# Optimization experiments

Hardware: AMD Instinct MI355X
Metric: run time of the kernel (lower is better)

## Reference

```python
import jax, jax.numpy as jnp
import numpy as np

WS = 8  # window/grid size, hard-coded in GlobalCirculationBlock
NH = 8  # num_heads


def _ln(x, w, b):
    m = jnp.mean(x, -1, keepdims=True)
    v = jnp.mean((x - m) ** 2, -1, keepdims=True)
    return (x - m) * jax.lax.rsqrt(v + 1e-5) * w + b


def _attn(q, k, v, scale):
    # q,k,v: [..., S, hd]
    s = jnp.einsum('...qd,...kd->...qk', q, k) * scale
    return jnp.einsum('...qk,...kd->...qd', jax.nn.softmax(s, axis=-1), v)


def setup_inputs() -> dict:
    key = jax.random.key(0)
    ks = jax.random.split(key, 8)
    B, C, H, W = 8, 128, 128, 128
    hid = 4 * C
    f = lambda k, shape, s=0.02: jax.random.normal(k, shape, jnp.float32) * s
    z = lambda n: jnp.zeros((n,), jnp.float32)
    return {
        'x': f(ks[0], (B, C, H, W), 1.0),
        'conv_w': f(ks[1], (C, 1, 3, 3)),        # depthwise 3x3 pos embed
        'conv_b': z(C),
        'norm1_w': jnp.ones((C,), jnp.float32), 'norm1_b': z(C),
        'wqkv': f(ks[2], (C, 3 * C)),            # qkv_bias=False
        'proj_w': f(ks[3], (C, C)), 'proj_b': z(C),
        'norm2_w': jnp.ones((C,), jnp.float32), 'norm2_b': z(C),
        'fc1_w': f(ks[4], (C, hid)), 'fc1_b': z(hid),
        'fc2_w': f(ks[5], (hid, C)), 'fc2_b': z(C),
        'ls1': jnp.full((C,), 1e-2, jnp.float32),
        'ls2': jnp.full((C,), 1e-2, jnp.float32),
    }


def reference(x, conv_w, conv_b, norm1_w, norm1_b, wqkv, proj_w, proj_b,
              norm2_w, norm2_b, fc1_w, fc1_b, fc2_w, fc2_b, ls1, ls2):
    B, C, H, W = x.shape
    nh, ws = NH, WS
    hd = C // nh
    scale = hd ** -0.5
    nhl = nh // 2                     # local heads == global heads
    nH, nW = H // ws, W // ws         # H,W multiples of ws -> no padding

    # depthwise conv positional embedding + residual
    pos = jax.lax.conv_general_dilated(
        x, conv_w, (1, 1), 'SAME',
        dimension_numbers=('NCHW', 'OIHW', 'NCHW'), feature_group_count=C)
    x = x + pos + conv_b[None, :, None, None]

    xt = x.reshape(B, C, H * W).transpose(0, 2, 1)   # [B, N, C]

    # ---- dual-scale attention ----
    xn = _ln(xt, norm1_w, norm1_b).reshape(B, H, W, C)
    qkv = (xn @ wqkv).reshape(B, H, W, 3, nh, hd)
    q, k, v = qkv[:, :, :, 0], qkv[:, :, :, 1], qkv[:, :, :, 2]  # [B,H,W,nh,hd]

    # local branch: first nhl heads, window attention (seq = ws*ws)
    def win(t):  # [B,H,W,nhl,hd] -> [B,nH,nW,nhl,ws*ws,hd]
        t = t.reshape(B, nH, ws, nW, ws, nhl, hd)
        return t.transpose(0, 1, 3, 5, 2, 4, 6).reshape(B, nH, nW, nhl, ws * ws, hd)

    ol = _attn(win(q[..., :nhl, :]), win(k[..., :nhl, :]), win(v[..., :nhl, :]), scale)
    ol = (ol.reshape(B, nH, nW, nhl, ws, ws, hd)
            .transpose(0, 1, 4, 2, 5, 3, 6)
            .reshape(B, H, W, nhl * hd))

    # global branch: last nhl heads, grid attention (seq = nH*nW)
    def grd(t):  # [B,H,W,nhl,hd] -> [B,ws,ws,nhl,nH*nW,hd]
        t = t.reshape(B, nH, ws, nW, ws, nhl, hd)
        return t.transpose(0, 2, 4, 5, 1, 3, 6).reshape(B, ws, ws, nhl, nH * nW, hd)

    og = _attn(grd(q[..., nhl:, :]), grd(k[..., nhl:, :]), grd(v[..., nhl:, :]), scale)
    og = (og.reshape(B, ws, ws, nhl, nH, nW, hd)
            .transpose(0, 4, 1, 5, 2, 3, 6)
            .reshape(B, H, W, nhl * hd))

    a = jnp.concatenate([ol, og], axis=-1).reshape(B, H * W, C)
    a = a @ proj_w + proj_b
    xt = xt + ls1 * a

    # ---- MLP ----
    h = _ln(xt, norm2_w, norm2_b)
    h = jax.nn.gelu(h @ fc1_w + fc1_b, approximate=False) @ fc2_w + fc2_b
    xt = xt + ls2 * h

    return xt.transpose(0, 2, 1).reshape(B, C, H, W)
```

## Files before the change

kernel.cpp:

```cpp
#include <hip/hip_runtime.h>
#include <hip/hip_bf16.h>

typedef __hip_bfloat16 bf16;
typedef __attribute__((ext_vector_type(8))) short short8;
typedef __attribute__((ext_vector_type(4))) short short4v;
typedef __attribute__((ext_vector_type(4))) float floatx4;
typedef __attribute__((ext_vector_type(16))) float floatx16;

#define Bn 8
#define Cc 128
#define Hh 128
#define Wl 128
#define HW (Hh*Wl)
#define NT (Bn*HW)
#define REG 8388608

#define QSCALE 0.36067376022224085f
#if __has_builtin(__builtin_amdgcn_exp2f)
#define EXP2(x) __builtin_amdgcn_exp2f(x)
#else
#define EXP2(x) __expf((x)*0.69314718055994531f)
#endif

__device__ __forceinline__ float b2f(bf16 v){ return __bfloat162float(v); }
__device__ __forceinline__ bf16  f2b(float v){ return __float2bfloat16(v); }

#define GL16(gp, lp) __builtin_amdgcn_global_load_lds( \
    (__attribute__((address_space(1))) unsigned int*)(gp), \
    (__attribute__((address_space(3))) unsigned int*)(lp), 16, 0, 0)

__global__ __launch_bounds__(256) void transpose_all(const float* __restrict__ wqkv,
                                                     const float* __restrict__ proj_w,
                                                     const float* __restrict__ fc1_w,
                                                     const float* __restrict__ fc2_w,
                                                     bf16* __restrict__ qkvT,
                                                     bf16* __restrict__ projT,
                                                     bf16* __restrict__ fc1T,
                                                     bf16* __restrict__ fc2T){
  int idx = blockIdx.x*256 + threadIdx.x;
  const float* src; bf16* dst; int K, N;
  if(idx < 49152){ src=wqkv; dst=qkvT; K=128; N=384; }
  else if(idx < 65536){ idx -= 49152; src=proj_w; dst=projT; K=128; N=128; }
  else if(idx < 131072){ idx -= 65536; src=fc1_w; dst=fc1T; K=128; N=512; }
  else { idx -= 131072; src=fc2_w; dst=fc2T; K=512; N=128; }
  int n = idx % N, k = idx / N;
  dst[(size_t)n*K + k] = f2b(src[idx]);
}

__global__ __launch_bounds__(256) void conv_kernel(const float* __restrict__ x,
                                                   const float* __restrict__ cw,
                                                   const float* __restrict__ cb,
                                                   float* __restrict__ xt){
  __shared__ float tile[16][132];
  int blk = blockIdx.x;
  int h = blk & 127; int t = blk >> 7;
  int cg = t & 7;    int b = t >> 3;
  int w4 = threadIdx.x & 31;
  int ci = threadIdx.x >> 5;
  int w0 = w4*4;
#pragma unroll
  for(int cc=0; cc<2; cc++){
    int c = cg*16 + ci*2 + cc;
    const float* xp = x + ((size_t)(b*Cc + c))*HW;
    float wg[9];
#pragma unroll
    for(int i=0;i<9;i++) wg[i] = cw[c*9+i];
    float4 rowv[3]; float lf[3], rt[3];
#pragma unroll
    for(int r=0;r<3;r++){
      int hh = h-1+r;
      float4 v = {0.f,0.f,0.f,0.f};
      if(hh>=0 && hh<Hh) v = *(const float4*)(xp + hh*Wl + w0);
      rowv[r] = v;
      float l = __shfl_up(v.w, 1, 32);
      float rr = __shfl_down(v.x, 1, 32);
      lf[r] = (w4==0)  ? 0.f : l;
      rt[r] = (w4==31) ? 0.f : rr;
    }
    float acc0 = cb[c], acc1 = cb[c], acc2 = cb[c], acc3 = cb[c];
#pragma unroll
    for(int r=0;r<3;r++){
      float4 v = rowv[r];
      acc0 += wg[r*3+0]*lf[r] + wg[r*3+1]*v.x + wg[r*3+2]*v.y;
      acc1 += wg[r*3+0]*v.x   + wg[r*3+1]*v.y + wg[r*3+2]*v.z;
      acc2 += wg[r*3+0]*v.y   + wg[r*3+1]*v.z + wg[r*3+2]*v.w;
      acc3 += wg[r*3+0]*v.z   + wg[r*3+1]*v.w + wg[r*3+2]*rt[r];
    }
    acc0 += rowv[1].x; acc1 += rowv[1].y; acc2 += rowv[1].z; acc3 += rowv[1].w;
    float4 o = {acc0, acc1, acc2, acc3};
    *(float4*)&tile[ci*2+cc][w0] = o;
  }
  __syncthreads();
  const size_t obase = ((size_t)b*HW + (size_t)h*Wl)*Cc + cg*16;
#pragma unroll
  for(int i=0;i<8;i++){
    int idx = i*256 + threadIdx.x;
    int c2 = idx & 15, w2 = idx >> 4;
    xt[obase + (size_t)w2*Cc + c2] = tile[c2][w2];
  }
}

__global__ __launch_bounds__(256) void ln_kernel(const float* __restrict__ xt,
                                                 const float* __restrict__ wv,
                                                 const float* __restrict__ bv,
                                                 bf16* __restrict__ xn){
  int tok  = blockIdx.x*4 + (threadIdx.x>>6);
  int lane = threadIdx.x & 63;
  const float* row = xt + (size_t)tok*Cc;
  float v0 = row[lane], v1 = row[lane+64];
  float s = v0+v1;
#pragma unroll
  for(int off=32; off; off>>=1) s += __shfl_down(s, off, 64);
  s = __shfl(s, 0, 64);
  float m = s * (1.0f/128.0f);
  float d0 = v0-m, d1 = v1-m;
  float vs = d0*d0 + d1*d1;
#pragma unroll
  for(int off=32; off; off>>=1) vs += __shfl_down(vs, off, 64);
  vs = __shfl(vs, 0, 64);
  float rstd = rsqrtf(vs*(1.0f/128.0f) + 1e-5f);
  bf16* orow = xn + (size_t)tok*Cc;
  orow[lane]    = f2b(d0*rstd*wv[lane]    + bv[lane]);
  orow[lane+64] = f2b(d1*rstd*wv[lane+64] + bv[lane+64]);
}

template<int EPI>
__global__ __launch_bounds__(256) void mfma_gemm(const bf16* __restrict__ A,
                                                 const bf16* __restrict__ Wt,
                                                 const float* __restrict__ bias,
                                                 bf16* __restrict__ outb,
                                                 float* __restrict__ xt,
                                                 const float* __restrict__ ls,
                                                 int N, int K){
  __shared__ short As[2][128*32];
  __shared__ short Bs[2][64*32];
  const int tid  = threadIdx.x;
  const int lane = tid & 63;
  const int w    = tid >> 6;

  const int nwg = gridDim.x * gridDim.y;
  const int lin = blockIdx.y * gridDim.x + blockIdx.x;
  const int t   = (lin & 7) * (nwg >> 3) + (lin >> 3);
  const int m0  = (t / gridDim.x) * 128;
  const int n0  = (t % gridDim.x) * 64;

  const int l1 = tid + 256;
  const bf16* gA0 = A  + (size_t)(m0 + ((tid>>6)<<4) + (tid&15))*K + (((tid>>4)&3)<<3);
  const bf16* gA1 = A  + (size_t)(m0 + ((l1 >>6)<<4) + (l1 &15))*K + (((l1 >>4)&3)<<3);
  const bf16* gB  = Wt + (size_t)(n0 + ((tid>>6)<<4) + (tid&15))*K + (((tid>>4)&3)<<3);
  const int ldsA0 = w*512;
  const int ldsA1 = 2048 + w*512;
  const int ldsB  = w*512;

  floatx4 acc[4][2];
#pragma unroll
  for(int i=0;i<4;i++)
#pragma unroll
    for(int j=0;j<2;j++) acc[i][j] = (floatx4){0.f,0.f,0.f,0.f};

  const int nk = K >> 5;
  GL16(gA0, &As[0][ldsA0]);
  GL16(gA1, &As[0][ldsA1]);
  GL16(gB , &Bs[0][ldsB ]);
  __syncthreads();

  int cur = 0;
  for(int it=0; it<nk; ++it){
    if(it+1 < nk){
      const int kn = (it+1) << 5;
      GL16(gA0 + kn, &As[cur^1][ldsA0]);
      GL16(gA1 + kn, &As[cur^1][ldsA1]);
      GL16(gB  + kn, &Bs[cur^1][ldsB ]);
    }
    short8 af[4], bfr[2];
#pragma unroll
    for(int mt=0;mt<4;mt++) af[mt] = *(short8*)&As[cur][(((w&1)*4+mt)*64 + lane)*8];
#pragma unroll
    for(int nt=0;nt<2;nt++) bfr[nt] = *(short8*)&Bs[cur][(((w>>1)*2+nt)*64 + lane)*8];
#pragma unroll
    for(int mt=0;mt<4;mt++)
#pragma unroll
      for(int nt=0;nt<2;nt++)
        acc[mt][nt] = __builtin_amdgcn_mfma_f32_16x16x32_bf16(af[mt], bfr[nt], acc[mt][nt], 0, 0, 0);
    __syncthreads();
    cur ^= 1;
  }

#pragma unroll
  for(int mt=0;mt<4;mt++){
#pragma unroll
    for(int nt=0;nt<2;nt++){
#pragma unroll
      for(int r=0;r<4;r++){
        int row = m0 + (w&1)*64 + mt*16 + ((lane>>4))*4 + r;
        int col = n0 + (w>>1)*32 + nt*16 + (lane&15);
        float v = acc[mt][nt][r];
        if(EPI==0){
          int reg = col >> 6;
          int head = (col >> 4) & 3;
          int ch = col & 15;
          int b = row >> 14, h = (row >> 7) & 127, ww = row & 127;
          if(reg < 2) v *= QSCALE;
          size_t didx;
          if(!(reg & 1)){
            int inst = ((b*16 + (h>>3))*16 + (ww>>3))*4 + head;
            int pos = (h&7)*8 + (ww&7);
            didx = ((size_t)inst*64 + pos)*16 + ch;
          } else {
            int inst = ((b*8 + (h&7))*8 + (ww&7))*4 + head;
            int pos = (h>>3)*16 + (ww>>3);
            didx = ((size_t)inst*256 + pos)*16 + ch;
          }
          outb[(size_t)reg*REG + didx] = f2b(v);
        } else if(EPI==1){
          v += bias[col];
          v = 0.5f*v*(1.0f + erff(v*0.70710678118f));
          outb[(size_t)row*N + col] = f2b(v);
        } else if(EPI==2){
          v += bias[col];
          xt[(size_t)row*128 + col] += ls[col]*v;
        } else {
          v += bias[col];
          float rr = xt[(size_t)row*128 + col] + ls[col]*v;
          outb[(size_t)row*128 + col] = f2b(rr);
        }
      }
    }
  }
}

__global__ __launch_bounds__(256) void attn_local2(const bf16* __restrict__ qL,
                                                   const bf16* __restrict__ kL,
                                                   const bf16* __restrict__ vL,
                                                   bf16* __restrict__ a){
  __shared__ short vt[16*72];
  __shared__ short pb[4][16*72];
  const int tid = threadIdx.x;
  const int w = tid >> 6, lane = tid & 63;
  const int n16 = lane & 15, quad = lane >> 4;
  const int blk = blockIdx.x;
  const int head = blk & 3, winid = blk >> 2;
  const bf16* Qb = qL + (size_t)blk*1024;
  const bf16* Kb = kL + (size_t)blk*1024;
  const bf16* Vb = vL + (size_t)blk*1024;

  if(tid < 128){
    int tok = tid >> 1, u = tid & 1;
    short8 v = *(const short8*)(Vb + tok*16 + u*8);
#pragma unroll
    for(int i=0;i<8;i++) vt[(u*8+i)*72 + tok] = ((short*)&v)[i];
  }
  __syncthreads();

  const int qt = w;
  short8 qf = {0,0,0,0,0,0,0,0};
  if(quad < 2) qf = *(const short8*)(Qb + (qt*16+n16)*16 + quad*8);

  floatx4 sf[4];
#pragma unroll
  for(int kt=0; kt<4; kt++){
    short8 kf = {0,0,0,0,0,0,0,0};
    if(quad < 2) kf = *(const short8*)(Kb + (kt*16+n16)*16 + quad*8);
    floatx4 z = (floatx4){0.f,0.f,0.f,0.f};
    sf[kt] = __builtin_amdgcn_mfma_f32_16x16x32_bf16(qf, kf, z, 0, 0, 0);
  }

  float mx[4] = {-1e30f,-1e30f,-1e30f,-1e30f};
#pragma unroll
  for(int kt=0; kt<4; kt++)
#pragma unroll
    for(int r=0;r<4;r++) mx[r] = fmaxf(mx[r], sf[kt][r]);
#pragma unroll
  for(int r=0;r<4;r++){
    mx[r] = fmaxf(mx[r], __shfl_xor(mx[r], 1, 64));
    mx[r] = fmaxf(mx[r], __shfl_xor(mx[r], 2, 64));
    mx[r] = fmaxf(mx[r], __shfl_xor(mx[r], 4, 64));
    mx[r] = fmaxf(mx[r], __shfl_xor(mx[r], 8, 64));
    mx[r] = -mx[r];
  }
  float l[4] = {0.f,0.f,0.f,0.f};
#pragma unroll
  for(int kt=0; kt<4; kt++){
#pragma unroll
    for(int r=0;r<4;r++){
      float p = EXP2(sf[kt][r] + mx[r]);
      l[r] += p;
      bf16 pbv = f2b(p);
      pb[w][(quad*4+r)*72 + kt*16 + n16] = *(short*)&pbv;
    }
  }
#pragma unroll
  for(int r=0;r<4;r++){
    l[r] += __shfl_xor(l[r], 1, 64);
    l[r] += __shfl_xor(l[r], 2, 64);
    l[r] += __shfl_xor(l[r], 4, 64);
    l[r] += __shfl_xor(l[r], 8, 64);
  }

  floatx4 of = (floatx4){0.f,0.f,0.f,0.f};
#pragma unroll
  for(int kb=0; kb<2; kb++){
    short8 pf = *(short8*)&pb[w][n16*72 + kb*32 + quad*8];
    short8 vfb = *(short8*)&vt[n16*72 + kb*32 + quad*8];
    of = __builtin_amdgcn_mfma_f32_16x16x32_bf16(pf, vfb, of, 0, 0, 0);
  }

  const int wj = winid & 15, wi = (winid >> 4) & 15, b = winid >> 8;
  const int ooff = head*16;
#pragma unroll
  for(int r=0;r<4;r++){
    int pos = qt*16 + quad*4 + r;
    int h = wi*8 + (pos>>3), ww = wj*8 + (pos&7);
    size_t t = (size_t)b*HW + (size_t)h*Wl + ww;
    a[t*Cc + ooff + n16] = f2b(of[r] / l[r]);
  }
}

__global__ __launch_bounds__(256) void attn_grid2(const bf16* __restrict__ qG,
                                                  const bf16* __restrict__ kG,
                                                  const bf16* __restrict__ vG,
                                                  bf16* __restrict__ a){
  __shared__ short vt[16*264];
  __shared__ short pb[4][32*136];
  const int tid = threadIdx.x;
  const int w = tid >> 6, lane = tid & 63;
  const int n16 = lane & 15, quad = lane >> 4;
  const int q32 = lane & 31, hb = lane >> 5;
  const int blk = blockIdx.x;
  const int head = blk & 3, ginst = blk >> 2;
  const bf16* Qb = qG + (size_t)blk*4096;
  const bf16* Kb = kG + (size_t)blk*4096;
  const bf16* Vb = vG + (size_t)blk*4096;

#pragma unroll
  for(int it=0; it<2; it++){
    int chunk = it*256 + tid;
    int tok = chunk >> 1, u = chunk & 1;
    short8 v = *(const short8*)(Vb + tok*16 + u*8);
#pragma unroll
    for(int i=0;i<8;i++) vt[(u*8+i)*264 + tok] = ((short*)&v)[i];
  }
  __syncthreads();

  const int sj = ginst & 7, si = (ginst >> 3) & 7, b = ginst >> 6;
  const int ooff = 64 + head*16;
  short* pbw = pb[w];
  const floatx16 Z16 = {0.f,0.f,0.f,0.f,0.f,0.f,0.f,0.f,0.f,0.f,0.f,0.f,0.f,0.f,0.f,0.f};

#pragma unroll
  for(int qi=0; qi<2; qi++){
    const int q0 = w*64 + qi*32;
    const short8 qf = *(const short8*)(Qb + (size_t)(q0 + q32)*16 + hb*8);
    float l_acc = 0.f;
    floatx4 of0 = (floatx4){0.f,0.f,0.f,0.f};
    floatx4 of1 = (floatx4){0.f,0.f,0.f,0.f};
#pragma unroll
    for(int kc=0; kc<2; kc++){
#pragma unroll
      for(int kt=0; kt<4; kt++){
        short8 kf = *(const short8*)(Kb + (size_t)(kc*128 + kt*32 + q32)*16 + hb*8);
        floatx16 s = __builtin_amdgcn_mfma_f32_32x32x16_bf16(kf, qf, Z16, 0, 0, 0);
#pragma unroll
        for(int g=0; g<4; g++){
          float p0 = EXP2(s[4*g+0]);
          float p1 = EXP2(s[4*g+1]);
          float p2 = EXP2(s[4*g+2]);
          float p3 = EXP2(s[4*g+3]);
          l_acc += (p0+p1)+(p2+p3);
          short4v pk = { (short)__bfloat16_as_ushort(f2b(p0)),
                         (short)__bfloat16_as_ushort(f2b(p1)),
                         (short)__bfloat16_as_ushort(f2b(p2)),
                         (short)__bfloat16_as_ushort(f2b(p3)) };
          *(short4v*)&pbw[q32*136 + kt*32 + g*8 + hb*4] = pk;
        }
      }
#pragma unroll
      for(int kb=0; kb<4; kb++){
        short8 vf  = *(short8*)&vt[n16*264 + kc*128 + kb*32 + quad*8];
        short8 pf0 = *(short8*)&pbw[n16*136 + kb*32 + quad*8];
        of0 = __builtin_amdgcn_mfma_f32_16x16x32_bf16(pf0, vf, of0, 0, 0, 0);
        short8 pf1 = *(short8*)&pbw[(16+n16)*136 + kb*32 + quad*8];
        of1 = __builtin_amdgcn_mfma_f32_16x16x32_bf16(pf1, vf, of1, 0, 0, 0);
      }
    }
    l_acc += __shfl_xor(l_acc, 32, 64);
#pragma unroll
    for(int hf=0; hf<2; hf++){
      floatx4 of = hf ? of1 : of0;
#pragma unroll
      for(int r=0;r<4;r++){
        float lr = __shfl(l_acc, hf*16 + quad*4 + r, 64);
        int pos = q0 + hf*16 + quad*4 + r;
        int h = (pos>>4)*8 + si, ww = (pos&15)*8 + sj;
        size_t t = (size_t)b*HW + (size_t)h*Wl + ww;
        a[t*Cc + ooff + n16] = f2b(of[r] / lr);
      }
    }
  }
}

__global__ __launch_bounds__(256) void transpose_kernel(const bf16* __restrict__ xf,
                                                        float* __restrict__ out){
  __shared__ bf16 tile[32][33];
  int t0 = blockIdx.x*32, c0 = blockIdx.y*32, b = blockIdx.z;
  int x = threadIdx.x, y = threadIdx.y;
  const bf16* src = xf + (size_t)b*HW*Cc;
  float* dst = out + (size_t)b*Cc*HW;
#pragma unroll
  for(int i=0;i<4;i++)
    tile[y*4+i][x] = src[(size_t)(t0 + y*4+i)*Cc + c0 + x];
  __syncthreads();
#pragma unroll
  for(int i=0;i<4;i++)
    dst[(size_t)(c0 + y*4+i)*HW + t0 + x] = b2f(tile[x][y*4+i]);
}

extern "C" void kernel_launch(void* const* d_in, const int* in_sizes, int n_in,
                              void* d_out, int out_size, void* d_ws, size_t ws_size,
                              hipStream_t stream) {
  const float* x       = (const float*)d_in[0];
  const float* conv_w  = (const float*)d_in[1];
  const float* conv_b  = (const float*)d_in[2];
  const float* norm1_w = (const float*)d_in[3];
  const float* norm1_b = (const float*)d_in[4];
  const float* wqkv    = (const float*)d_in[5];
  const float* proj_w  = (const float*)d_in[6];
  const float* proj_b  = (const float*)d_in[7];
  const float* norm2_w = (const float*)d_in[8];
  const float* norm2_b = (const float*)d_in[9];
  const float* fc1_w   = (const float*)d_in[10];
  const float* fc1_b   = (const float*)d_in[11];
  const float* fc2_w   = (const float*)d_in[12];
  const float* fc2_b   = (const float*)d_in[13];
  const float* ls1     = (const float*)d_in[14];
  const float* ls2     = (const float*)d_in[15];
  float* out = (float*)d_out;

  char* ws = (char*)d_ws;
  float* xt = (float*)ws;
  bf16*  sh = (bf16*)(ws + (size_t)NT*Cc*4);
  bf16*  qh = (bf16*)(ws + (size_t)NT*Cc*4 + (size_t)NT*Cc*2);
  bf16*  wt = (bf16*)(ws + (size_t)NT*Cc*4 + (size_t)NT*Cc*2 + (size_t)NT*512*2);
  bf16* qkvT = wt;
  bf16* projT= wt + 49152;
  bf16* fc1T = wt + 65536;
  bf16* fc2T = wt + 131072;

  transpose_all<<<196608/256, 256, 0, stream>>>(wqkv, proj_w, fc1_w, fc2_w,
                                                qkvT, projT, fc1T, fc2T);
  conv_kernel<<<Bn*8*Hh, 256, 0, stream>>>(x, conv_w, conv_b, xt);
  ln_kernel<<<NT/4, 256, 0, stream>>>(xt, norm1_w, norm1_b, sh);
  mfma_gemm<0><<<dim3(384/64, NT/128), 256, 0, stream>>>(sh, qkvT, nullptr, qh, nullptr, nullptr, 384, 128);
  attn_grid2<<<2048, 256, 0, stream>>>(qh + (size_t)1*REG, qh + (size_t)3*REG, qh + (size_t)5*REG, sh);
  attn_local2<<<8192, 256, 0, stream>>>(qh + (size_t)0*REG, qh + (size_t)2*REG, qh + (size_t)4*REG, sh);
  mfma_gemm<2><<<dim3(128/64, NT/128), 256, 0, stream>>>(sh, projT, proj_b, nullptr, xt, ls1, 128, 128);
  ln_kernel<<<NT/4, 256, 0, stream>>>(xt, norm2_w, norm2_b, sh);
  mfma_gemm<1><<<dim3(512/64, NT/128), 256, 0, stream>>>(sh, fc1T, fc1_b, qh, nullptr, nullptr, 512, 128);
  mfma_gemm<3><<<dim3(128/64, NT/128), 256, 0, stream>>>(qh, fc2T, fc2_b, sh, xt, ls2, 128, 512);
  transpose_kernel<<<dim3(HW/32, Cc/32, Bn), dim3(32,8), 0, stream>>>(sh, out);
}
```

Measured before the change: 468.8 us.

## Fuse fc1, GELU and fc2 into one MLP kernel keeping hidden in LDS

Replaces the separate fc1+GELU and fc2+residual GEMM launches with one kernel. Each block keeps its 128-row A tile in registers, computes 64-column chunks of the hidden activation into shared memory, and accumulates fc2 immediately. This avoids writing and re-reading the 512-wide hidden tensor through global memory. It also swaps exact erf GELU for a tanh-style approximation using exp2, which adds small numerical error.

```diff
diff --git a/kernel.cpp b/kernel.cpp
--- a/kernel.cpp
+++ b/kernel.cpp
@@ -212,18 +212,123 @@
             didx = ((size_t)inst*256 + pos)*16 + ch;
           }
           outb[(size_t)reg*REG + didx] = f2b(v);
-        } else if(EPI==1){
-          v += bias[col];
-          v = 0.5f*v*(1.0f + erff(v*0.70710678118f));
-          outb[(size_t)row*N + col] = f2b(v);
         } else if(EPI==2){
           v += bias[col];
           xt[(size_t)row*128 + col] += ls[col]*v;
-        } else {
-          v += bias[col];
-          float rr = xt[(size_t)row*128 + col] + ls[col]*v;
-          outb[(size_t)row*128 + col] = f2b(rr);
         }
+      }
+    }
+  }
+}
+
+__global__ __launch_bounds__(256) void fused_mlp(const bf16* A,
+                                                 const bf16* __restrict__ W1,
+                                                 const float* __restrict__ b1,
+                                                 const bf16* __restrict__ W2,
+                                                 const float* __restrict__ b2,
+                                                 const float* __restrict__ xt,
+                                                 const float* __restrict__ ls,
+                                                 bf16* outb){
+  __shared__ short W1s[16*512];
+  __shared__ short W2s[16*512];
+  __shared__ short hs[4][32*72];
+  const int tid = threadIdx.x, lane = tid & 63, w = tid >> 6;
+  const int n16 = lane & 15, quad = lane >> 4;
+  const int lin = blockIdx.x;
+  const int t = (lin & 7)*128 + (lin >> 3);
+  const int m0 = t*128;
+  const int mw = m0 + w*32;
+
+  short8 areg[2][4];
+#pragma unroll
+  for(int mt=0;mt<2;mt++)
+#pragma unroll
+    for(int ks=0;ks<4;ks++)
+      areg[mt][ks] = *(const short8*)(A + (size_t)(mw + mt*16 + n16)*128 + ks*32 + quad*8);
+
+  floatx4 acc2[2][8];
+#pragma unroll
+  for(int i=0;i<2;i++)
+#pragma unroll
+    for(int j=0;j<8;j++) acc2[i][j] = (floatx4){0.f,0.f,0.f,0.f};
+
+  short* hw = hs[w];
+
+  for(int nc=0; nc<8; ++nc){
+    if(nc) __syncthreads();
+#pragma unroll
+    for(int p=0;p<4;p++){
+      int fid = p*4 + w;
+      int nt = fid >> 2, ks = fid & 3;
+      const bf16* s1 = W1 + (size_t)(nc*64 + nt*16 + n16)*128 + ks*32 + quad*8;
+      GL16(s1, &W1s[fid*512]);
+      int nt2 = fid >> 1, ks2 = fid & 1;
+      const bf16* s2 = W2 + (size_t)(nt2*16 + n16)*512 + nc*64 + ks2*32 + quad*8;
+      GL16(s2, &W2s[fid*512]);
+    }
+    __syncthreads();
+
+    floatx4 acc1[2][4];
+#pragma unroll
+    for(int i=0;i<2;i++)
+#pragma unroll
+      for(int j=0;j<4;j++) acc1[i][j] = (floatx4){0.f,0.f,0.f,0.f};
+#pragma unroll
+    for(int ks=0;ks<4;ks++){
+      short8 bfr[4];
+#pragma unroll
+      for(int nt=0;nt<4;nt++) bfr[nt] = *(short8*)&W1s[(nt*4+ks)*512 + lane*8];
+#pragma unroll
+      for(int mt=0;mt<2;mt++)
+#pragma unroll
+        for(int nt=0;nt<4;nt++)
+          acc1[mt][nt] = __builtin_amdgcn_mfma_f32_16x16x32_bf16(areg[mt][ks], bfr[nt], acc1[mt][nt], 0, 0, 0);
+    }
+
+#pragma unroll
+    for(int nt=0;nt<4;nt++){
+      float bb = b1[nc*64 + nt*16 + n16];
+#pragma unroll
+      for(int mt=0;mt<2;mt++){
+#pragma unroll
+        for(int r=0;r<4;r++){
+          float v = acc1[mt][nt][r] + bb;
+          float u = v*v;
+          float e = EXP2(v*__fmaf_rn(u, 0.044715f, 1.0f)*(-2.3022127f));
+          float g = v*__frcp_rn(1.0f + e);
+          bf16 gb = f2b(g);
+          hw[(mt*16 + quad*4 + r)*72 + nt*16 + n16] = *(short*)&gb;
+        }
+      }
+    }
+
+#pragma unroll
+    for(int ks2=0;ks2<2;ks2++){
+      short8 ha[2];
+#pragma unroll
+      for(int mt=0;mt<2;mt++) ha[mt] = *(short8*)&hw[(mt*16 + n16)*72 + ks2*32 + quad*8];
+#pragma unroll
+      for(int nt2=0;nt2<8;nt2++){
+        short8 bf2 = *(short8*)&W2s[(nt2*2+ks2)*512 + lane*8];
+#pragma unroll
+        for(int mt=0;mt<2;mt++)
+          acc2[mt][nt2] = __builtin_amdgcn_mfma_f32_16x16x32_bf16(ha[mt], bf2, acc2[mt][nt2], 0, 0, 0);
+      }
+    }
+  }
+
+#pragma unroll
+  for(int nt2=0;nt2<8;nt2++){
+    int col = nt2*16 + n16;
+    float bb = b2[col], lsv = ls[col];
+#pragma unroll
+    for(int mt=0;mt<2;mt++){
+#pragma unroll
+      for(int r=0;r<4;r++){
+        int row = mw + mt*16 + quad*4 + r;
+        float v = acc2[mt][nt2][r] + bb;
+        float rr = xt[(size_t)row*128 + col] + lsv*v;
+        outb[(size_t)row*128 + col] = f2b(rr);
       }
     }
   }
@@ -455,7 +560,6 @@
   attn_local2<<<8192, 256, 0, stream>>>(qh + (size_t)0*REG, qh + (size_t)2*REG, qh + (size_t)4*REG, sh);
   mfma_gemm<2><<<dim3(128/64, NT/128), 256, 0, stream>>>(sh, projT, proj_b, nullptr, xt, ls1, 128, 128);
   ln_kernel<<<NT/4, 256, 0, stream>>>(xt, norm2_w, norm2_b, sh);
-  mfma_gemm<1><<<dim3(512/64, NT/128), 256, 0, stream>>>(sh, fc1T, fc1_b, qh, nullptr, nullptr, 512, 128);
-  mfma_gemm<3><<<dim3(128/64, NT/128), 256, 0, stream>>>(qh, fc2T, fc2_b, sh, xt, ls2, 128, 512);
+  fused_mlp<<<NT/128, 256, 0, stream>>>(sh, fc1T, fc1_b, fc2T, fc2_b, xt, ls2, sh);
   transpose_kernel<<<dim3(HW/32, Cc/32, Bn), dim3(32,8), 0, stream>>>(sh, out);
 }
```

After: 457.1 us. -2.5%, faster.
